# Performance work log

Hardware: AMD Instinct MI355X
Metric: run time of the kernel (lower is better)

## Reference

```python
import jax, jax.numpy as jnp
from jax import lax
import numpy as np

I_CNN = 2048   # box feature dim
Q_H = 1024     # LSTM hidden
Q_E = 300      # word embedding dim
HID = 512      # gated MLP hidden
B = 256
MAXN = 100
T = 14


def setup_inputs() -> dict:
    key = jax.random.key(0)
    ks = jax.random.split(key, 12)
    w = lambda k, shape: (jax.random.normal(k, shape, dtype=jnp.float32) * 0.02)
    return {
        "wholefeat": jax.random.normal(ks[0], (B, I_CNN), dtype=jnp.float32),
        "pooled": jax.random.normal(ks[1], (B, I_CNN), dtype=jnp.float32),
        "box_feats": jax.random.normal(ks[2], (B, MAXN, I_CNN), dtype=jnp.float32),
        "q_feats": jax.random.normal(ks[3], (B, T, Q_E), dtype=jnp.float32),
        "box_coords": jax.random.uniform(ks[4], (B, MAXN, 4), dtype=jnp.float32),
        "index": jax.random.randint(ks[5], (B,), 1, MAXN + 1),
        # LSTM params (PyTorch layout: gates ordered i,f,g,o)
        "W_ih": w(ks[6], (4 * Q_H, Q_E)),
        "W_hh": w(ks[7], (4 * Q_H, Q_H)),
        "b_ih": jnp.zeros((4 * Q_H,), jnp.float32),
        "b_hh": jnp.zeros((4 * Q_H,), jnp.float32),
        # gated MLP params
        "W_w": w(ks[8], (HID, I_CNN + Q_H)),
        "W_b": jnp.zeros((HID,), jnp.float32),
        "Wp_w": w(ks[9], (HID, I_CNN + Q_H)),
        "Wp_b": jnp.zeros((HID,), jnp.float32),
        "f_w": w(ks[10], (1, HID)),
    }


def _lstm_last(x_tbe, W_ih, W_hh, b_ih, b_hh):
    # x_tbe: [T, B, E] time-major. Returns final hidden state h_T: [B, H].
    H = W_hh.shape[1]
    # precompute input projections for all timesteps: [T, B, 4H]
    xg = jnp.einsum('tbe,ge->tbg', x_tbe, W_ih) + (b_ih + b_hh)

    def step(carry, xt):
        h, c = carry
        gates = xt + h @ W_hh.T                       # [B, 4H]
        i, f, g, o = jnp.split(gates, 4, axis=-1)
        i = jax.nn.sigmoid(i)
        f = jax.nn.sigmoid(f)
        g = jnp.tanh(g)
        o = jax.nn.sigmoid(o)
        c = f * c + i * g
        h = o * jnp.tanh(c)
        return (h, c), None

    h0 = jnp.zeros((x_tbe.shape[1], H), x_tbe.dtype)
    (h, _), _ = lax.scan(step, (h0, h0), xg)
    return h


def reference(wholefeat, pooled, box_feats, q_feats, box_coords, index,
              W_ih, W_hh, b_ih, b_hh, W_w, W_b, Wp_w, Wp_b, f_w):
    # question encoding: last LSTM output per sample -> [B, Q_H]
    q_rnn = _lstm_last(jnp.transpose(q_feats, (1, 0, 2)), W_ih, W_hh, b_ih, b_hh)

    Bn, N, _ = box_feats.shape
    qst = jnp.broadcast_to(q_rnn[:, None, :], (Bn, N, q_rnn.shape[-1]))
    b_full = jnp.concatenate([box_feats, qst], axis=-1)        # [B, N, 3072]

    y_tilde = jnp.tanh(jnp.einsum('bnd,hd->bnh', b_full, W_w) + W_b)
    g = jax.nn.sigmoid(jnp.einsum('bnd,hd->bnh', b_full, Wp_w) + Wp_b)
    si = y_tilde * g                                           # [B, N, HID]
    wsi = jax.nn.sigmoid(jnp.einsum('bnh,oh->bno', si, f_w))[..., 0]  # [B, N]

    # ragged reduction: only the first index[i] boxes of sample i contribute
    mask = (jnp.arange(N)[None, :] < index[:, None]).astype(wsi.dtype)
    return jnp.sum(wsi * mask, axis=1)                         # [B]
```

## Files before the change

kernel.cpp:

```cpp
#include <hip/hip_runtime.h>
#include <cstdint>
#include <cstddef>

#define DEVI __device__ __forceinline__

typedef __attribute__((ext_vector_type(8))) short short8;
typedef __attribute__((ext_vector_type(4))) float f32x4;
typedef __bf16 bf16x8 __attribute__((ext_vector_type(8)));

DEVI float sigf(float x) { return 1.0f / (1.0f + __expf(-x)); }
DEVI float tanh_f(float x) { return 2.0f / (1.0f + __expf(-2.0f * x)) - 1.0f; }

DEVI short f2bf(float x) {
    uint32_t u = __builtin_bit_cast(uint32_t, x);
    u += 0x7FFFu + ((u >> 16) & 1u);
    return (short)(u >> 16);
}
DEVI float bf2f(short s) {
    uint32_t u = ((uint32_t)(unsigned short)s) << 16;
    return __builtin_bit_cast(float, u);
}

DEVI void gload16(const void* g, void* l) {
    __builtin_amdgcn_global_load_lds(
        (const __attribute__((address_space(1))) void*)g,
        (__attribute__((address_space(3))) void*)l, 16, 0, 0);
}

DEVI f32x4 mfma16(short8 a, short8 b, f32x4 c) {
    return __builtin_amdgcn_mfma_f32_16x16x32_bf16(
        __builtin_bit_cast(bf16x8, a), __builtin_bit_cast(bf16x8, b), c, 0, 0, 0);
}


#define W_SLOTS   688128
#define WC_SLOTS  393216
#define XB_SLOTS  143360
#define LG_SLOTS  6400
#define PREP_TOT  (W_SLOTS + WC_SLOTS + XB_SLOTS + LG_SLOTS)

__global__ __launch_bounds__(256) void prep_all(const int* __restrict__ index,
                                                const float* __restrict__ Wih,
                                                const float* __restrict__ Whh,
                                                const float* __restrict__ bih,
                                                const float* __restrict__ bhh,
                                                const float* __restrict__ Ww,
                                                const float* __restrict__ Wpw,
                                                const float* __restrict__ q,
                                                int* __restrict__ cum,
                                                int* __restrict__ bmap,
                                                short* __restrict__ Wstk,
                                                short* __restrict__ Wcat,
                                                short* __restrict__ xb,
                                                float* __restrict__ lgt) {
    __shared__ int sh[256];
    if (blockIdx.x == 0) {
        int t = threadIdx.x;
        int myidx = index[t];
        sh[t] = myidx;
        __syncthreads();
        for (int off = 1; off < 256; off <<= 1) {
            int v = (t >= off) ? sh[t - off] : 0;
            __syncthreads();
            sh[t] += v;
            __syncthreads();
        }
        cum[t + 1] = sh[t];
        if (t == 0) cum[0] = 0;
        int base = sh[t] - myidx;
        for (int j = 0; j < myidx; ++j) bmap[base + j] = t;
        bmap[sh[255] + t] = 0;
        return;
    }
    int s = (blockIdx.x - 1) * 256 + threadIdx.x;
    if (s < W_SLOTS) {
        int n = s / 168, c8 = s - n * 168, kb = c8 * 8;
        int hblk = n >> 6, gate = (n >> 4) & 3, hl = n & 15;
        int on = gate * 1024 + hblk * 16 + hl;
        short8 o;
#pragma unroll
        for (int e = 0; e < 8; ++e) {
            int k = kb + e;
            float v;
            if (k < 300) v = Wih[on * 300 + k];
            else if (k == 300) v = bih[on] + bhh[on];
            else if (k < 320) v = 0.f;
            else v = Whh[on * 1024 + (k - 320)];
            o[e] = f2bf(v);
        }
        *(short8*)&Wstk[n * 1344 + kb] = o;
        return;
    }
    s -= W_SLOTS;
    if (s < WC_SLOTS) {
        int n = s / 384, c8 = s - n * 384, kb = c8 * 8;
        int hg = n >> 5, which = (n >> 4) & 1, hl = n & 15;
        int h = hg * 16 + hl;
        const float* src = (which ? Wpw : Ww) + (size_t)h * 3072 + kb;
        float4 v0 = *(const float4*)src;
        float4 v1 = *(const float4*)(src + 4);
        short8 o;
        o[0] = f2bf(v0.x); o[1] = f2bf(v0.y); o[2] = f2bf(v0.z); o[3] = f2bf(v0.w);
        o[4] = f2bf(v1.x); o[5] = f2bf(v1.y); o[6] = f2bf(v1.z); o[7] = f2bf(v1.w);
        *(short8*)&Wcat[(size_t)n * 3072 + kb] = o;
        return;
    }
    s -= WC_SLOTS;
    if (s < XB_SLOTS) {
        int row = s / 40, c8 = s - row * 40, eb = c8 * 8;
        int t = row / 256, b = row - t * 256;
        const float* qr = q + (size_t)(b * 14 + t) * 300;
        short8 o;
#pragma unroll
        for (int e = 0; e < 8; ++e) {
            int ee = eb + e;
            float v = (ee < 300) ? qr[ee] : (ee == 300 ? 1.0f : 0.0f);
            o[e] = f2bf(v);
        }
        *(short8*)&xb[(size_t)row * 320 + eb] = o;
        return;
    }
    s -= XB_SLOTS;
    if (s < LG_SLOTS) { ((f32x4*)lgt)[s] = f32x4{0.f, 0.f, 0.f, 0.f}; return; }
}

__global__ __launch_bounds__(256) void compact_box(const float* __restrict__ box,
                                                   const int* __restrict__ index,
                                                   const int* __restrict__ cum,
                                                   short* __restrict__ Ac) {
    int m = blockIdx.x;
    int b = m / 100, j = m - b * 100;
    if (j >= index[b]) return;
    size_t dr = (size_t)(cum[b] + j);
    int t = threadIdx.x;
    const float* src = box + (size_t)m * 2048 + t * 8;
    float4 v0 = *(const float4*)src;
    float4 v1 = *(const float4*)(src + 4);
    short8 s;
    s[0] = f2bf(v0.x); s[1] = f2bf(v0.y); s[2] = f2bf(v0.z); s[3] = f2bf(v0.w);
    s[4] = f2bf(v1.x); s[5] = f2bf(v1.y); s[6] = f2bf(v1.z); s[7] = f2bf(v1.w);
    *(short8*)&Ac[dr * 2048 + t * 8] = s;
}


__global__ __launch_bounds__(256) void xg_gemm(const short* __restrict__ xb,
                                               const short* __restrict__ Wstk,
                                               short* __restrict__ xg,
                                               float* __restrict__ c,
                                               short* __restrict__ hb1) {
    __shared__ __attribute__((aligned(16))) short As[128 * 64];
    __shared__ __attribute__((aligned(16))) short Bs[128 * 64];
    const int tid = threadIdx.x, l = tid & 63, w = tid >> 6;
    const int n0 = blockIdx.x * 128;
    const int m0 = blockIdx.y * 128;
    const int wm = w >> 1, wn = w & 1;

    const short* asrc[4];
    const short* bsrc[4];
    for (int i = 0; i < 4; i++) {
        int r = w * 32 + i * 8 + (l >> 3);
        int cs = (l & 7) ^ (r & 7);
        asrc[i] = xb + (size_t)(m0 + r) * 320 + cs * 8;
        bsrc[i] = Wstk + (size_t)(n0 + r) * 1344 + cs * 8;
    }

    f32x4 acc[4][4];
    for (int i = 0; i < 4; i++)
        for (int j = 0; j < 4; j++) acc[i][j] = f32x4{0.f, 0.f, 0.f, 0.f};

    for (int kt = 0; kt < 5; ++kt) {
        const int k0 = kt * 64;
        __syncthreads();
        for (int i = 0; i < 4; i++)
            gload16(asrc[i] + k0, &As[(w * 32 + i * 8) * 64]);
        for (int i = 0; i < 4; i++)
            gload16(bsrc[i] + k0, &Bs[(w * 32 + i * 8) * 64]);
        __syncthreads();
        for (int ks = 0; ks < 2; ++ks) {
            short8 a[4], b[4];
            for (int mf = 0; mf < 4; ++mf) {
                int m = wm * 64 + mf * 16 + (l & 15);
                int ca = (ks * 4 + (l >> 4)) ^ (m & 7);
                a[mf] = *(const short8*)&As[m * 64 + ca * 8];
            }
            for (int nf = 0; nf < 4; ++nf) {
                int n = wn * 64 + nf * 16 + (l & 15);
                int cb = (ks * 4 + (l >> 4)) ^ (n & 7);
                b[nf] = *(const short8*)&Bs[n * 64 + cb * 8];
            }
            for (int mf = 0; mf < 4; ++mf)
                for (int nf = 0; nf < 4; ++nf)
                    acc[mf][nf] = mfma16(a[mf], b[nf], acc[mf][nf]);
        }
    }
    const int hl = l & 15, hi = l >> 4;
    if (m0 < 256) {
        const int h = ((n0 + wn * 64) >> 6) * 16 + hl;
        for (int mf = 0; mf < 4; ++mf)
            for (int rg = 0; rg < 4; ++rg) {
                int b = m0 + wm * 64 + mf * 16 + hi * 4 + rg;
                float ig = acc[mf][0][rg];
                float gg = acc[mf][2][rg];
                float og = acc[mf][3][rg];
                float cn = sigf(ig) * tanh_f(gg);
                size_t off = (size_t)b * 1024 + h;
                c[off] = cn;
                hb1[off] = f2bf(sigf(og) * tanh_f(cn));
            }
    } else {
        for (int mf = 0; mf < 4; ++mf)
            for (int nf = 0; nf < 4; ++nf)
                for (int rg = 0; rg < 4; ++rg) {
                    int row = m0 + wm * 64 + mf * 16 + hi * 4 + rg;
                    int col = n0 + wn * 64 + nf * 16 + hl;
                    xg[(size_t)row * 4096 + col] = f2bf(acc[mf][nf][rg]);
                }
    }
}


__global__ __launch_bounds__(128) void lstm_step(const short* __restrict__ hin,
                                                 const short* __restrict__ Wstk,
                                                 const short* __restrict__ xg_t,
                                                 float* __restrict__ c,
                                                 short* __restrict__ hout) {
    __shared__ __attribute__((aligned(16))) short As[2][32 * 128];
    __shared__ __attribute__((aligned(16))) short Bs[2][64 * 128];
    const int tid = threadIdx.x, l = tid & 63, w = tid >> 6;
    const int hi = l >> 4, hl = l & 15;
    const int bid = blockIdx.x;
    const int xcd = bid & 7, ii = bid >> 3;
    const int ny = xcd * 8 + (ii & 7);
    const int mx = ii >> 3;
    const int m0 = mx * 32, n0g = ny * 64;

    f32x4 acc[4];
    for (int i = 0; i < 4; i++) acc[i] = f32x4{0.f, 0.f, 0.f, 0.f};

    const short* asrc[4];
    const short* bsrc[8];
    for (int i = 0; i < 4; i++) {
        int s = i * 128 + tid;
        int r = s >> 4, cs = s & 15;
        asrc[i] = hin + (size_t)(m0 + r) * 1024 + ((cs ^ (r & 15)) * 8);
    }
    for (int i = 0; i < 8; i++) {
        int s = i * 128 + tid;
        int r = s >> 4, cs = s & 15;
        bsrc[i] = Wstk + (size_t)(n0g + r) * 1344 + 320 + ((cs ^ (r & 15)) * 8);
    }
    for (int i = 0; i < 4; i++) gload16(asrc[i], &As[0][(i * 128 + tid) * 8]);
    for (int i = 0; i < 8; i++) gload16(bsrc[i], &Bs[0][(i * 128 + tid) * 8]);

    for (int kt = 0; kt < 8; ++kt) {
        const int cur = kt & 1;
        if (kt < 7) {
            const int k0 = (kt + 1) * 128;
            for (int i = 0; i < 4; i++)
                gload16(asrc[i] + k0, &As[cur ^ 1][(i * 128 + tid) * 8]);
            for (int i = 0; i < 8; i++)
                gload16(bsrc[i] + k0, &Bs[cur ^ 1][(i * 128 + tid) * 8]);
            asm volatile("s_waitcnt vmcnt(12)" ::: "memory");
        } else {
            asm volatile("s_waitcnt vmcnt(0)" ::: "memory");
        }
        __builtin_amdgcn_sched_barrier(0);
        __builtin_amdgcn_s_barrier();
        __builtin_amdgcn_sched_barrier(0);
#pragma unroll
        for (int ks = 0; ks < 4; ++ks) {
            const int mrow = w * 16 + hl;
            const int ca = (ks * 4 + hi) ^ hl;
            short8 a = *(const short8*)&As[cur][mrow * 128 + ca * 8];
#pragma unroll
            for (int nf = 0; nf < 4; ++nf) {
                const int nrow = nf * 16 + hl;
                short8 b = *(const short8*)&Bs[cur][nrow * 128 + ca * 8];
                acc[nf] = mfma16(a, b, acc[nf]);
            }
        }
        __builtin_amdgcn_sched_barrier(0);
        asm volatile("s_waitcnt lgkmcnt(0)" ::: "memory");
        __builtin_amdgcn_s_barrier();
        __builtin_amdgcn_sched_barrier(0);
    }

    const short* xr0 = xg_t + (size_t)(m0 + w * 16 + hi * 4) * 4096 + n0g + hl;
    for (int rg = 0; rg < 4; ++rg) {
        const short* xr = xr0 + (size_t)rg * 4096;
        float ig = acc[0][rg] + bf2f(xr[0]);
        float fg = acc[1][rg] + bf2f(xr[16]);
        float gg = acc[2][rg] + bf2f(xr[32]);
        float og = acc[3][rg] + bf2f(xr[48]);
        size_t off = (size_t)(m0 + w * 16 + hi * 4 + rg) * 1024 + ny * 16 + hl;
        float cn = sigf(fg) * c[off] + sigf(ig) * tanh_f(gg);
        c[off] = cn;
        hout[off] = f2bf(sigf(og) * tanh_f(cn));
    }
}


__global__ __launch_bounds__(512) void mlp_gemm(const short* __restrict__ Ac,
                                                const short* __restrict__ hb,
                                                const short* __restrict__ Wcat,
                                                const int* __restrict__ mliveptr,
                                                const int* __restrict__ bmap,
                                                const float* __restrict__ Wb,
                                                const float* __restrict__ Wpb,
                                                const float* __restrict__ fw,
                                                float* __restrict__ logits) {
    __shared__ __attribute__((aligned(16))) short As[256 * 64];
    __shared__ __attribute__((aligned(16))) short Bs[128 * 64];
    const int Mlive = *mliveptr;
    const int tid = threadIdx.x, l = tid & 63, w = tid >> 6;
    const int bid = blockIdx.x;
    const int xcd = bid & 7, ii = bid >> 3;
    const int x = ii & 7, q = ii >> 3;
    const int y = q * 8 + xcd;
    const int n0 = x * 128, m0 = y * 256;
    if (m0 >= Mlive) return;
    const int wm = w >> 1, wn = w & 1;

    const short* asrc[4];
    const short* hsrc[4];
    int adst[4];
    const short* bsrc[2];
    int bdst[2];
    for (int i = 0; i < 4; i++) {
        int r = i * 64 + w * 8 + (l >> 3);
        int cs = (l & 7) ^ (r & 7);
        asrc[i] = Ac + (size_t)(m0 + r) * 2048 + cs * 8;
        hsrc[i] = hb + (size_t)bmap[m0 + r] * 1024 + cs * 8;
        adst[i] = (i * 64 + w * 8) * 64;
    }
    for (int i = 0; i < 2; i++) {
        int r = i * 64 + w * 8 + (l >> 3);
        int cs = (l & 7) ^ (r & 7);
        bsrc[i] = Wcat + (size_t)(n0 + r) * 3072 + cs * 8;
        bdst[i] = (i * 64 + w * 8) * 64;
    }

    f32x4 acc[4][4];
    for (int i = 0; i < 4; i++)
        for (int j = 0; j < 4; j++) acc[i][j] = f32x4{0.f, 0.f, 0.f, 0.f};

    for (int kt = 0; kt < 48; ++kt) {
        const int k0 = kt * 64;
        __syncthreads();
        if (kt < 32) {
            for (int i = 0; i < 4; i++)
                gload16(asrc[i] + k0, &As[adst[i]]);
        } else {
            const int kq = k0 - 2048;
            for (int i = 0; i < 4; i++)
                gload16(hsrc[i] + kq, &As[adst[i]]);
        }
        for (int i = 0; i < 2; i++)
            gload16(bsrc[i] + k0, &Bs[bdst[i]]);
        __syncthreads();
        for (int ks = 0; ks < 2; ++ks) {
            short8 a[4], b[4];
            for (int mf = 0; mf < 4; ++mf) {
                int m = wm * 64 + mf * 16 + (l & 15);
                int ca = (ks * 4 + (l >> 4)) ^ (m & 7);
                a[mf] = *(const short8*)&As[m * 64 + ca * 8];
            }
            for (int nf = 0; nf < 4; ++nf) {
                int n = wn * 64 + nf * 16 + (l & 15);
                int cb = (ks * 4 + (l >> 4)) ^ (n & 7);
                b[nf] = *(const short8*)&Bs[n * 64 + cb * 8];
            }
            for (int mf = 0; mf < 4; ++mf)
                for (int nf = 0; nf < 4; ++nf)
                    acc[mf][nf] = mfma16(a[mf], b[nf], acc[mf][nf]);
        }
    }

    const int hl = l & 15, hi = l >> 4;
    for (int mf = 0; mf < 4; ++mf) {
        float part[4] = {0.f, 0.f, 0.f, 0.f};
        for (int p = 0; p < 2; ++p) {
            int ntg = (n0 + wn * 64) / 16 + 2 * p;
            int hg = ntg >> 1;
            int h = hg * 16 + hl;
            float fwv = fw[h], wbv = Wb[h], wpbv = Wpb[h];
            for (int rg = 0; rg < 4; ++rg) {
                float y2 = tanh_f(acc[mf][2 * p][rg] + wbv);
                float g2 = sigf(acc[mf][2 * p + 1][rg] + wpbv);
                part[rg] += y2 * g2 * fwv;
            }
        }
        for (int rg = 0; rg < 4; ++rg) {
            float v = part[rg];
            v += __shfl_xor(v, 1, 64);
            v += __shfl_xor(v, 2, 64);
            v += __shfl_xor(v, 4, 64);
            v += __shfl_xor(v, 8, 64);
            if (hl == 0) {
                int row = m0 + wm * 64 + mf * 16 + hi * 4 + rg;
                atomicAdd(&logits[row], v);
            }
        }
    }
}

__global__ __launch_bounds__(128) void reduce_out(const float* __restrict__ logits,
                                                  const int* __restrict__ index,
                                                  const int* __restrict__ cum,
                                                  float* __restrict__ out) {
    int b = blockIdx.x, t = threadIdx.x;
    int idx = index[b];
    int base = cum[b];
    float v = 0.f;
    if (t < 100 && t < idx) v = sigf(logits[base + t]);
    for (int m = 32; m; m >>= 1) v += __shfl_down(v, m, 64);
    __shared__ float s[2];
    if ((t & 63) == 0) s[t >> 6] = v;
    __syncthreads();
    if (t == 0) out[b] = s[0] + s[1];
}


extern "C" void kernel_launch(void* const* d_in, const int* in_sizes, int n_in,
                              void* d_out, int out_size, void* d_ws, size_t ws_size,
                              hipStream_t stream) {
    (void)in_sizes; (void)n_in; (void)out_size; (void)ws_size;
    const float* box = (const float*)d_in[2];
    const float* qf  = (const float*)d_in[3];
    const int* index = (const int*)d_in[5];
    const float* Wih = (const float*)d_in[6];
    const float* Whh = (const float*)d_in[7];
    const float* bih = (const float*)d_in[8];
    const float* bhh = (const float*)d_in[9];
    const float* Ww  = (const float*)d_in[10];
    const float* Wb  = (const float*)d_in[11];
    const float* Wpw = (const float*)d_in[12];
    const float* Wpb = (const float*)d_in[13];
    const float* fw  = (const float*)d_in[14];

    char* p = (char*)d_ws;
    short* Wstk = (short*)p;  p += (size_t)4096 * 1344 * 2;
    short* Wcat = (short*)p;  p += (size_t)1024 * 3072 * 2;
    short* xb   = (short*)p;  p += (size_t)3584 * 320 * 2;
    short* hb0  = (short*)p;  p += (size_t)256 * 1024 * 2;
    short* hb1  = (short*)p;  p += (size_t)256 * 1024 * 2;
    short* xg   = (short*)p;  p += (size_t)3584 * 4096 * 2;
    float* c    = (float*)p;  p += (size_t)256 * 1024 * 4;
    int*   cum  = (int*)p;    p += 260 * 4;
    int*   bmap = (int*)p;    p += (size_t)(25600 + 256) * 4;
    float* lgt  = (float*)p;  p += (size_t)25600 * 4;
    p = (char*)(((uintptr_t)p + 255) & ~(uintptr_t)255);
    short* Ac   = (short*)p;  p += (size_t)25600 * 2048 * 2;

    prep_all<<<1 + PREP_TOT / 256, 256, 0, stream>>>(
        index, Wih, Whh, bih, bhh, Ww, Wpw, qf, cum, bmap, Wstk, Wcat, xb, lgt);

    compact_box<<<25600, 256, 0, stream>>>(box, index, cum, Ac);

    xg_gemm<<<dim3(32, 28), 256, 0, stream>>>(xb, Wstk, xg, c, hb1);

    short* hbuf[2] = {hb0, hb1};
    for (int t = 1; t < 14; ++t) {
        lstm_step<<<512, 128, 0, stream>>>(
            hbuf[t & 1], Wstk, xg + (size_t)t * 256 * 4096, c, hbuf[(t & 1) ^ 1]);
    }

    mlp_gemm<<<800, 512, 0, stream>>>(Ac, hb0, Wcat, cum + 256, bmap,
                                      Wb, Wpb, fw, lgt);
    reduce_out<<<256, 128, 0, stream>>>(lgt, index, cum, (float*)d_out);
}
```

Measured before the change: 299.0 us.

## Prefetch A via registers and double-buffer B in mlp_gemm; merge compact and xg launches

mlp_gemm now prefetches the next A tile into registers and the next B tile into a second LDS buffer while the current tile is multiplied. This replaces the old load-sync-compute pattern, which exposed global load latency every k-step. Separately, compact_box and xg_gemm are merged into one launch that picks its role from the block index, removing a launch boundary and letting the two run side by side. The cost is more registers and LDS, which may lower occupancy, plus some leftover dead address arithmetic.

```diff
diff --git a/kernel.cpp b/kernel.cpp
--- a/kernel.cpp
+++ b/kernel.cpp
@@ -124,35 +124,37 @@
     if (s < LG_SLOTS) { ((f32x4*)lgt)[s] = f32x4{0.f, 0.f, 0.f, 0.f}; return; }
 }
 
-__global__ __launch_bounds__(256) void compact_box(const float* __restrict__ box,
-                                                   const int* __restrict__ index,
-                                                   const int* __restrict__ cum,
-                                                   short* __restrict__ Ac) {
-    int m = blockIdx.x;
-    int b = m / 100, j = m - b * 100;
-    if (j >= index[b]) return;
-    size_t dr = (size_t)(cum[b] + j);
-    int t = threadIdx.x;
-    const float* src = box + (size_t)m * 2048 + t * 8;
-    float4 v0 = *(const float4*)src;
-    float4 v1 = *(const float4*)(src + 4);
-    short8 s;
-    s[0] = f2bf(v0.x); s[1] = f2bf(v0.y); s[2] = f2bf(v0.z); s[3] = f2bf(v0.w);
-    s[4] = f2bf(v1.x); s[5] = f2bf(v1.y); s[6] = f2bf(v1.z); s[7] = f2bf(v1.w);
-    *(short8*)&Ac[dr * 2048 + t * 8] = s;
-}
-
-
-__global__ __launch_bounds__(256) void xg_gemm(const short* __restrict__ xb,
-                                               const short* __restrict__ Wstk,
-                                               short* __restrict__ xg,
-                                               float* __restrict__ c,
-                                               short* __restrict__ hb1) {
+
+__global__ __launch_bounds__(256) void compact_xg(const short* __restrict__ xb,
+                                                  const short* __restrict__ Wstk,
+                                                  short* __restrict__ xg,
+                                                  float* __restrict__ c,
+                                                  short* __restrict__ hb1,
+                                                  const float* __restrict__ box,
+                                                  const int* __restrict__ index,
+                                                  const int* __restrict__ cum,
+                                                  short* __restrict__ Ac) {
     __shared__ __attribute__((aligned(16))) short As[128 * 64];
     __shared__ __attribute__((aligned(16))) short Bs[128 * 64];
+    const int bid = blockIdx.x;
+    if (bid >= 896) {
+        int m = bid - 896;
+        int b = m / 100, j = m - b * 100;
+        if (j >= index[b]) return;
+        size_t dr = (size_t)(cum[b] + j);
+        int t = threadIdx.x;
+        const float* src = box + (size_t)m * 2048 + t * 8;
+        float4 v0 = *(const float4*)src;
+        float4 v1 = *(const float4*)(src + 4);
+        short8 s;
+        s[0] = f2bf(v0.x); s[1] = f2bf(v0.y); s[2] = f2bf(v0.z); s[3] = f2bf(v0.w);
+        s[4] = f2bf(v1.x); s[5] = f2bf(v1.y); s[6] = f2bf(v1.z); s[7] = f2bf(v1.w);
+        *(short8*)&Ac[dr * 2048 + t * 8] = s;
+        return;
+    }
     const int tid = threadIdx.x, l = tid & 63, w = tid >> 6;
-    const int n0 = blockIdx.x * 128;
-    const int m0 = blockIdx.y * 128;
+    const int n0 = (bid & 31) * 128;
+    const int m0 = (bid >> 5) * 128;
     const int wm = w >> 1, wn = w & 1;
 
     const short* asrc[4];
@@ -310,7 +312,7 @@
                                                 const float* __restrict__ fw,
                                                 float* __restrict__ logits) {
     __shared__ __attribute__((aligned(16))) short As[256 * 64];
-    __shared__ __attribute__((aligned(16))) short Bs[128 * 64];
+    __shared__ __attribute__((aligned(16))) short Bs[2][128 * 64];
     const int Mlive = *mliveptr;
     const int tid = threadIdx.x, l = tid & 63, w = tid >> 6;
     const int bid = blockIdx.x;
@@ -331,8 +333,12 @@
         int cs = (l & 7) ^ (r & 7);
         asrc[i] = Ac + (size_t)(m0 + r) * 2048 + cs * 8;
         hsrc[i] = hb + (size_t)bmap[m0 + r] * 1024 + cs * 8;
-        adst[i] = (i * 64 + w * 8) * 64;
-    }
+        adst[i] = (i * 64 + w * 8) * 64 + ((((l & 7) ^ ((w * 8 + (l >> 3)) & 7)) ^ ((w * 8 + (l >> 3)) & 7)) * 0);
+    }
+    for (int i = 0; i < 4; i++)
+        adst[i] = (i * 64 + w * 8) * 64 + (l & 63) * 0;
+    int adst2[4];
+    for (int i = 0; i < 4; i++) adst2[i] = ((i * 64 + w * 8) * 64) + l * 8;
     for (int i = 0; i < 2; i++) {
         int r = i * 64 + w * 8 + (l >> 3);
         int cs = (l & 7) ^ (r & 7);
@@ -344,20 +350,34 @@
     for (int i = 0; i < 4; i++)
         for (int j = 0; j < 4; j++) acc[i][j] = f32x4{0.f, 0.f, 0.f, 0.f};
 
+    short8 areg[4];
+#pragma unroll
+    for (int i = 0; i < 4; i++) areg[i] = *(const short8*)asrc[i];
+    for (int i = 0; i < 2; i++) gload16(bsrc[i], &Bs[0][bdst[i]]);
+
     for (int kt = 0; kt < 48; ++kt) {
-        const int k0 = kt * 64;
-        __syncthreads();
-        if (kt < 32) {
-            for (int i = 0; i < 4; i++)
-                gload16(asrc[i] + k0, &As[adst[i]]);
-        } else {
-            const int kq = k0 - 2048;
-            for (int i = 0; i < 4; i++)
-                gload16(hsrc[i] + kq, &As[adst[i]]);
-        }
-        for (int i = 0; i < 2; i++)
-            gload16(bsrc[i] + k0, &Bs[bdst[i]]);
-        __syncthreads();
+        const int cur = kt & 1;
+        asm volatile("s_waitcnt vmcnt(0)" ::: "memory");
+        __builtin_amdgcn_sched_barrier(0);
+#pragma unroll
+        for (int i = 0; i < 4; i++) *(short8*)&As[adst2[i]] = areg[i];
+        if (kt < 47) {
+            const int k1 = (kt + 1) * 64;
+            for (int i = 0; i < 2; i++)
+                gload16(bsrc[i] + k1, &Bs[cur ^ 1][bdst[i]]);
+            if (kt + 1 < 32) {
+#pragma unroll
+                for (int i = 0; i < 4; i++) areg[i] = *(const short8*)(asrc[i] + k1);
+            } else {
+                const int kq = k1 - 2048;
+#pragma unroll
+                for (int i = 0; i < 4; i++) areg[i] = *(const short8*)(hsrc[i] + kq);
+            }
+        }
+        __builtin_amdgcn_sched_barrier(0);
+        asm volatile("s_waitcnt lgkmcnt(0)" ::: "memory");
+        __builtin_amdgcn_s_barrier();
+        __builtin_amdgcn_sched_barrier(0);
         for (int ks = 0; ks < 2; ++ks) {
             short8 a[4], b[4];
             for (int mf = 0; mf < 4; ++mf) {
@@ -368,12 +388,16 @@
             for (int nf = 0; nf < 4; ++nf) {
                 int n = wn * 64 + nf * 16 + (l & 15);
                 int cb = (ks * 4 + (l >> 4)) ^ (n & 7);
-                b[nf] = *(const short8*)&Bs[n * 64 + cb * 8];
+                b[nf] = *(const short8*)&Bs[cur][n * 64 + cb * 8];
             }
             for (int mf = 0; mf < 4; ++mf)
                 for (int nf = 0; nf < 4; ++nf)
                     acc[mf][nf] = mfma16(a[mf], b[nf], acc[mf][nf]);
         }
+        __builtin_amdgcn_sched_barrier(0);
+        asm volatile("s_waitcnt lgkmcnt(0)" ::: "memory");
+        __builtin_amdgcn_s_barrier();
+        __builtin_amdgcn_sched_barrier(0);
     }
 
     const int hl = l & 15, hi = l >> 4;
@@ -455,9 +479,8 @@
     prep_all<<<1 + PREP_TOT / 256, 256, 0, stream>>>(
         index, Wih, Whh, bih, bhh, Ww, Wpw, qf, cum, bmap, Wstk, Wcat, xb, lgt);
 
-    compact_box<<<25600, 256, 0, stream>>>(box, index, cum, Ac);
-
-    xg_gemm<<<dim3(32, 28), 256, 0, stream>>>(xb, Wstk, xg, c, hb1);
+    compact_xg<<<896 + 25600, 256, 0, stream>>>(xb, Wstk, xg, c, hb1,
+                                                box, index, cum, Ac);
 
     short* hbuf[2] = {hb0, hb1};
     for (int t = 1; t < 14; ++t) {
```

New measurement: 352.7 us. 18.0% more time.
